# Kernel optimization log

Hardware: AMD Instinct MI355X
Metric: run time of the kernel (lower is better)

The kernel has to match this reference:

```python
import jax, jax.numpy as jnp
import numpy as np

N_NODES = 100000


def setup_inputs() -> dict:
    key = jax.random.key(0)
    k1, k2, k3, k4 = jax.random.split(key, 4)
    E = 1600000
    D_IN, D_OUT = 128, 128
    feat = jax.random.normal(k1, (N_NODES, D_IN), dtype=jnp.float32)
    src = jax.random.randint(k2, (E,), 0, N_NODES, dtype=jnp.int32)
    dst = jax.random.randint(k3, (E,), 0, N_NODES, dtype=jnp.int32)
    # xavier_uniform for weight [in, out]
    limit = float(np.sqrt(6.0 / (D_IN + D_OUT)))
    weight = jax.random.uniform(k4, (D_IN, D_OUT), dtype=jnp.float32,
                                minval=-limit, maxval=limit)
    bias = jnp.zeros((D_OUT,), dtype=jnp.float32)
    return {"feat": feat, "weight": weight, "bias": bias, "src": src, "dst": dst}


def reference(feat, weight, bias, src, dst):
    # in-degree normalization: norm_i = 1/sqrt(in_deg(i)); clamp deg>=1 to avoid inf
    deg = jax.ops.segment_sum(jnp.ones(src.shape[0], dtype=jnp.float32), dst,
                              num_segments=N_NODES)
    norm = jax.lax.rsqrt(jnp.maximum(deg, 1.0))[:, None]  # [N,1]
    h = feat * norm
    # update_all(copy_src, sum): scatter-sum src features into dst nodes (SpMM)
    agg = jax.ops.segment_sum(h[src], dst, num_segments=N_NODES)  # [N, D_in]
    # in_feats == out_feats -> aggregate first, then dense transform
    rst = agg @ weight          # [N, D_out]
    rst = rst * norm + bias
    return rst
```

## Files before the change

kernel.cpp:

```cpp
#include <hip/hip_runtime.h>


constexpr int N_NODES = 100000;
constexpr int D = 128;
constexpr int NB = 256;
constexpr int GROUP = (N_NODES + NB - 1) / NB;
constexpr int CAP = 14336;

typedef float f32x4 __attribute__((ext_vector_type(4)));
typedef short short8 __attribute__((ext_vector_type(8)));
typedef unsigned uint4v __attribute__((ext_vector_type(4)));

__device__ __forceinline__ ushort f2bf(float x) {
    unsigned u = __float_as_uint(x);
    return (ushort)((u + 0x7fffu + ((u >> 16) & 1u)) >> 16);
}
__device__ __forceinline__ float bf2f(ushort h) {
    return __uint_as_float(((unsigned)h) << 16);
}

__global__ __launch_bounds__(256) void p1_histo(const int* __restrict__ dst, int E,
                                                int* __restrict__ bhist) {
    __shared__ int h[NB];
    int t = threadIdx.x, blk = blockIdx.x;
    h[t] = 0; __syncthreads();
    int per = (E + NB - 1) / NB;
    int s = blk * per, e = min(E, s + per);
    for (int i = s + t; i < e; i += 256) atomicAdd(&h[dst[i] / GROUP], 1);
    __syncthreads();
    bhist[t * NB + blk] = h[t];
}

__global__ __launch_bounds__(256) void p1_scanrow(int* __restrict__ bhist,
                                                  int* __restrict__ rowtot) {
    __shared__ int lds[256];
    int b = blockIdx.x, t = threadIdx.x;
    int v = bhist[b * NB + t];
    lds[t] = v; __syncthreads();
    for (int off = 1; off < 256; off <<= 1) {
        int x = (t >= off) ? lds[t - off] : 0;
        __syncthreads();
        lds[t] += x;
        __syncthreads();
    }
    bhist[b * NB + t] = lds[t] - v;
    if (t == 255) rowtot[b] = lds[255];
}

__global__ __launch_bounds__(256) void p1_scantot(const int* __restrict__ rowtot,
                                                  int* __restrict__ bktBase) {
    __shared__ int lds[256];
    int t = threadIdx.x;
    int v = rowtot[t];
    lds[t] = v; __syncthreads();
    for (int off = 1; off < 256; off <<= 1) {
        int x = (t >= off) ? lds[t - off] : 0;
        __syncthreads();
        lds[t] += x;
        __syncthreads();
    }
    bktBase[t] = lds[t] - v;
    if (t == 255) bktBase[NB] = lds[255];
}

__global__ __launch_bounds__(256) void p1_scatter(const int* __restrict__ src,
                                                  const int* __restrict__ dst, int E,
                                                  const int* __restrict__ bhist,
                                                  const int* __restrict__ bktBase,
                                                  int* __restrict__ pairs) {
    __shared__ int loff[NB];
    int t = threadIdx.x, blk = blockIdx.x;
    loff[t] = bhist[t * NB + blk] + bktBase[t]; __syncthreads();
    int per = (E + NB - 1) / NB;
    int s = blk * per, e = min(E, s + per);
    for (int i = s + t; i < e; i += 256) {
        int d = dst[i];
        int b = d / GROUP;
        int pos = atomicAdd(&loff[b], 1);
        pairs[pos] = ((d - b * GROUP) << 17) | src[i];
    }
}

__global__ __launch_bounds__(256) void p2_degoffs(const int* __restrict__ pairs,
                                                  const int* __restrict__ bktBase,
                                                  int* __restrict__ deg,
                                                  int* __restrict__ offs,
                                                  float* __restrict__ norm) {
    __shared__ int h[512];
    __shared__ int ssum[256];
    int t = threadIdx.x, b = blockIdx.x;
    int lo = b * GROUP;
    int cnt = min(GROUP, N_NODES - lo);
    for (int i = t; i < 512; i += 256) h[i] = 0;
    __syncthreads();
    int s0 = bktBase[b], s1 = bktBase[b + 1];
    for (int i = s0 + t; i < s1; i += 256) atomicAdd(&h[pairs[i] >> 17], 1);
    __syncthreads();
    int v0 = h[2 * t], v1 = h[2 * t + 1];
    int s = v0 + v1;
    ssum[t] = s; __syncthreads();
    for (int off = 1; off < 256; off <<= 1) {
        int x = (t >= off) ? ssum[t - off] : 0;
        __syncthreads();
        ssum[t] += x;
        __syncthreads();
    }
    int pre = ssum[t] - s;
    if (2 * t < cnt) {
        int node = lo + 2 * t;
        deg[node] = v0;
        offs[node] = s0 + pre;
        norm[node] = rsqrtf(fmaxf((float)v0, 1.0f));
    }
    if (2 * t + 1 < cnt) {
        int node = lo + 2 * t + 1;
        deg[node] = v1;
        offs[node] = s0 + pre + v0;
        norm[node] = rsqrtf(fmaxf((float)v1, 1.0f));
    }
}

__global__ __launch_bounds__(256) void p2_scatter(const int* __restrict__ pairs,
                                                  const int* __restrict__ bktBase,
                                                  const int* __restrict__ offs, int E,
                                                  int* __restrict__ esrc) {
    __shared__ int loffs[GROUP];
    __shared__ int lcur[GROUP];
    __shared__ int sbuf[CAP];
    int t = threadIdx.x, b = blockIdx.x;
    int lo = b * GROUP;
    int cnt = min(GROUP, N_NODES - lo);
    int base = bktBase[b];
    int end  = bktBase[b + 1];
    int wsize = end - base;
    for (int i = t; i < cnt; i += 256) { loffs[i] = offs[lo + i] - base; lcur[i] = 0; }
    __syncthreads();
    bool fits = (wsize <= CAP);
    for (int i = base + t; i < end; i += 256) {
        int p = pairs[i];
        int dl = p >> 17;
        int sv = p & 0x1FFFF;
        int pos = loffs[dl] + atomicAdd(&lcur[dl], 1);
        if (fits) sbuf[pos] = sv; else esrc[base + pos] = sv;
    }
    __syncthreads();
    if (fits)
        for (int i = t; i < wsize; i += 256) esrc[base + i] = sbuf[i];
}

__global__ void k_featbf(const float* __restrict__ feat, const float* __restrict__ norm,
                         unsigned* __restrict__ ft, int total) {
    int i = blockIdx.x * blockDim.x + threadIdx.x;
    if (i < total) {
        float w = norm[i >> 6];
        float2 v = ((const float2*)feat)[i];
        ft[i] = (unsigned)f2bf(v.x * w) | ((unsigned)f2bf(v.y * w) << 16);
    }
}

template<bool OUT_BF>
__global__ __launch_bounds__(256) void k_gather4(const unsigned* __restrict__ ft,
                                                 const int* __restrict__ offs,
                                                 const int* __restrict__ deg,
                                                 const int* __restrict__ esrc,
                                                 void* __restrict__ out) {
    int gtid = blockIdx.x * blockDim.x + threadIdx.x;
    int node = gtid >> 6;
    if (node >= N_NODES) return;
    int lane = gtid & 63;
    int g  = lane >> 4;
    int sl = lane & 15;
    int start = offs[node];
    int cnt   = deg[node];
    int last  = start + cnt - 1;
    float acc[8] = {0.f, 0.f, 0.f, 0.f, 0.f, 0.f, 0.f, 0.f};
    const uint4v* ftv = (const uint4v*)ft;
    for (int j = 0; j < cnt; j += 4) {
        int idx = start + j + g;
        int s = esrc[min(idx, last)];
        float w = (j + g < cnt) ? 1.0f : 0.0f;
        uint4v u = ftv[(size_t)s * 16 + sl];
        #pragma unroll
        for (int q = 0; q < 4; ++q) {
            unsigned uu = u[q];
            acc[q * 2]     = fmaf(__uint_as_float(uu << 16),          w, acc[q * 2]);
            acc[q * 2 + 1] = fmaf(__uint_as_float(uu & 0xffff0000u),  w, acc[q * 2 + 1]);
        }
    }
    #pragma unroll
    for (int q = 0; q < 8; ++q) {
        acc[q] += __shfl_xor(acc[q], 16, 64);
        acc[q] += __shfl_xor(acc[q], 32, 64);
    }
    if (OUT_BF) {
        if (g == 0) {
            uint4v o;
            #pragma unroll
            for (int q = 0; q < 4; ++q)
                o[q] = (unsigned)f2bf(acc[q * 2]) | ((unsigned)f2bf(acc[q * 2 + 1]) << 16);
            ((uint4v*)out)[(size_t)node * 16 + sl] = o;
        }
    } else {
        float2 o = {acc[g * 2], acc[g * 2 + 1]};
        ((float2*)out)[(size_t)node * 64 + sl * 4 + g] = o;
    }
}

__global__ __launch_bounds__(256) void k_gather(const float* __restrict__ feat,
                                                const float* __restrict__ norm,
                                                const int* __restrict__ offs,
                                                const int* __restrict__ deg,
                                                const int* __restrict__ esrc,
                                                float* __restrict__ agg) {
    int gtid = blockIdx.x * blockDim.x + threadIdx.x;
    int node = gtid >> 6;
    int lane = gtid & 63;
    if (node >= N_NODES) return;
    int start = offs[node];
    int cnt   = deg[node];
    float2 acc = {0.f, 0.f};
    const float2* feat2 = (const float2*)feat;
    int j = 0;
    for (; j + 2 <= cnt; j += 2) {
        int s0 = esrc[start + j];
        int s1 = esrc[start + j + 1];
        float n0 = norm[s0], n1 = norm[s1];
        float2 v0 = feat2[(size_t)s0 * 64 + lane];
        float2 v1 = feat2[(size_t)s1 * 64 + lane];
        acc.x = fmaf(v0.x, n0, acc.x); acc.y = fmaf(v0.y, n0, acc.y);
        acc.x = fmaf(v1.x, n1, acc.x); acc.y = fmaf(v1.y, n1, acc.y);
    }
    if (j < cnt) {
        int s0 = esrc[start + j];
        float n0 = norm[s0];
        float2 v0 = feat2[(size_t)s0 * 64 + lane];
        acc.x = fmaf(v0.x, n0, acc.x); acc.y = fmaf(v0.y, n0, acc.y);
    }
    ((float2*)agg)[(size_t)node * 64 + lane] = acc;
}

__global__ void k_wpack(const float* __restrict__ W, ushort* __restrict__ whi,
                        ushort* __restrict__ wlo) {
    int p = blockIdx.x * blockDim.x + threadIdx.x;
    if (p >= 16384) return;
    int i  = p & 7;
    int l  = (p >> 3) & 63;
    int kt = (p >> 9) & 3;
    int ct = (p >> 11);
    int k = kt * 32 + (l >> 4) * 8 + i;
    int n = ct * 16 + (l & 15);
    float x = W[k * 128 + n];
    ushort h = f2bf(x);
    whi[p] = h;
    wlo[p] = f2bf(x - bf2f(h));
}

__global__ __launch_bounds__(256) void k_gemm_bf(const ushort* __restrict__ aggbf,
                                                 const ushort* __restrict__ whi,
                                                 const ushort* __restrict__ wlo,
                                                 const float* __restrict__ bias,
                                                 const float* __restrict__ norm,
                                                 float* __restrict__ out) {
    __shared__ ushort sH[16384];
    __shared__ ushort sL[16384];
    {
        const short8* gh = (const short8*)whi;
        const short8* gl = (const short8*)wlo;
        short8* lh = (short8*)sH;
        short8* ll = (short8*)sL;
        for (int i = threadIdx.x; i < 2048; i += 256) { lh[i] = gh[i]; ll[i] = gl[i]; }
    }
    __syncthreads();

    const int lane = threadIdx.x & 63;
    const int wid  = threadIdx.x >> 6;
    const int rsub = lane & 15;
    const int kgrp = lane >> 4;

    const short8* BH = (const short8*)sH;
    const short8* BL = (const short8*)sL;

    const int nstrips = N_NODES / 16;
    for (int strip = blockIdx.x * 4 + wid; strip < nstrips; strip += gridDim.x * 4) {
        const int row0 = strip * 16;
        const ushort* arow = aggbf + (size_t)(row0 + rsub) * D + kgrp * 8;
        short8 a[4];
        #pragma unroll
        for (int kt = 0; kt < 4; ++kt) a[kt] = *(const short8*)(arow + kt * 32);
        float nr[4];
        #pragma unroll
        for (int r = 0; r < 4; ++r) nr[r] = norm[row0 + kgrp * 4 + r];

        #pragma unroll
        for (int ct = 0; ct < 8; ++ct) {
            f32x4 acc = {0.f, 0.f, 0.f, 0.f};
            #pragma unroll
            for (int kt = 0; kt < 4; ++kt) {
                acc = __builtin_amdgcn_mfma_f32_16x16x32_bf16(a[kt], BH[(ct * 4 + kt) * 64 + lane], acc, 0, 0, 0);
                acc = __builtin_amdgcn_mfma_f32_16x16x32_bf16(a[kt], BL[(ct * 4 + kt) * 64 + lane], acc, 0, 0, 0);
            }
            const float bc = bias[ct * 16 + rsub];
            float* ocol = out + (size_t)row0 * D + ct * 16 + rsub;
            #pragma unroll
            for (int r = 0; r < 4; ++r) {
                int row = kgrp * 4 + r;
                ocol[(size_t)row * D] = acc[r] * nr[r] + bc;
            }
        }
    }
}

__global__ __launch_bounds__(256) void k_gemm_mfma(float* __restrict__ io,
                                                   const ushort* __restrict__ whi,
                                                   const ushort* __restrict__ wlo,
                                                   const float* __restrict__ bias,
                                                   const float* __restrict__ norm) {
    __shared__ ushort sH[16384];
    __shared__ ushort sL[16384];
    {
        const short8* gh = (const short8*)whi;
        const short8* gl = (const short8*)wlo;
        short8* lh = (short8*)sH;
        short8* ll = (short8*)sL;
        for (int i = threadIdx.x; i < 2048; i += 256) { lh[i] = gh[i]; ll[i] = gl[i]; }
    }
    __syncthreads();

    const int lane = threadIdx.x & 63;
    const int wid  = threadIdx.x >> 6;
    const int rsub = lane & 15;
    const int kgrp = lane >> 4;

    const short8* BH = (const short8*)sH;
    const short8* BL = (const short8*)sL;

    const int nstrips = N_NODES / 16;
    for (int strip = blockIdx.x * 4 + wid; strip < nstrips; strip += gridDim.x * 4) {
        const int row0 = strip * 16;
        const float* arow = io + (size_t)(row0 + rsub) * D + kgrp * 8;
        short8 ahi[4], alo[4];
        #pragma unroll
        for (int kt = 0; kt < 4; ++kt) {
            f32x4 x0 = *(const f32x4*)(arow + kt * 32);
            f32x4 x1 = *(const f32x4*)(arow + kt * 32 + 4);
            short8 h, l;
            #pragma unroll
            for (int j = 0; j < 4; ++j) {
                ushort h0 = f2bf(x0[j]);
                h[j]     = (short)h0;  l[j]     = (short)f2bf(x0[j] - bf2f(h0));
                ushort h1 = f2bf(x1[j]);
                h[j + 4] = (short)h1;  l[j + 4] = (short)f2bf(x1[j] - bf2f(h1));
            }
            ahi[kt] = h; alo[kt] = l;
        }
        float nr[4];
        #pragma unroll
        for (int r = 0; r < 4; ++r) nr[r] = norm[row0 + kgrp * 4 + r];

        #pragma unroll
        for (int ct = 0; ct < 8; ++ct) {
            f32x4 acc = {0.f, 0.f, 0.f, 0.f};
            #pragma unroll
            for (int kt = 0; kt < 4; ++kt) {
                short8 bh = BH[(ct * 4 + kt) * 64 + lane];
                short8 bl = BL[(ct * 4 + kt) * 64 + lane];
                acc = __builtin_amdgcn_mfma_f32_16x16x32_bf16(ahi[kt], bh, acc, 0, 0, 0);
                acc = __builtin_amdgcn_mfma_f32_16x16x32_bf16(alo[kt], bh, acc, 0, 0, 0);
                acc = __builtin_amdgcn_mfma_f32_16x16x32_bf16(ahi[kt], bl, acc, 0, 0, 0);
            }
            const float bc = bias[ct * 16 + rsub];
            float* ocol = io + (size_t)row0 * D + ct * 16 + rsub;
            #pragma unroll
            for (int r = 0; r < 4; ++r) {
                int row = kgrp * 4 + r;
                ocol[(size_t)row * D] = acc[r] * nr[r] + bc;
            }
        }
    }
}

__global__ void k_scatter(const float* __restrict__ feat, const int* __restrict__ src,
                          const int* __restrict__ dst, const float* __restrict__ norm,
                          int E, float* __restrict__ agg) {
    long long gtid = (long long)blockIdx.x * blockDim.x + threadIdx.x;
    int e    = (int)(gtid >> 6);
    int lane = (int)(gtid & 63);
    if (e >= E) return;
    int s = src[e];
    int t = dst[e];
    float ns = norm[s];
    float2 v = ((const float2*)(feat + (size_t)s * D))[lane];
    float* arow = agg + (size_t)t * D + lane * 2;
    atomicAdd(arow + 0, v.x * ns);
    atomicAdd(arow + 1, v.y * ns);
}
__global__ void k_deg_f(const int* __restrict__ dst, int E, float* __restrict__ deg) {
    int i = blockIdx.x * blockDim.x + threadIdx.x;
    if (i < E) atomicAdd(deg + dst[i], 1.0f);
}
__global__ void k_norm_f(float* __restrict__ dn) {
    int i = blockIdx.x * blockDim.x + threadIdx.x;
    if (i < N_NODES) dn[i] = rsqrtf(fmaxf(dn[i], 1.0f));
}
__global__ __launch_bounds__(256) void k_gemm(float* __restrict__ io,
                                              const float* __restrict__ W,
                                              const float* __restrict__ bias,
                                              const float* __restrict__ norm) {
    __shared__ float sW[D * D];
    __shared__ float srow[2][D];
    for (int i = threadIdx.x; i < D * D; i += 256) sW[i] = W[i];
    const int r = threadIdx.x >> 7;
    const int c = threadIdx.x & 127;
    const float bc = bias[c];
    const int npairs = N_NODES / 2;
    for (int rp = blockIdx.x; rp < npairs; rp += gridDim.x) {
        __syncthreads();
        const int row = rp * 2 + r;
        srow[r][c] = io[(size_t)row * D + c];
        __syncthreads();
        float acc = 0.f;
        #pragma unroll 8
        for (int k = 0; k < D; ++k)
            acc = fmaf(srow[r][k], sW[k * D + c], acc);
        io[(size_t)row * D + c] = acc * norm[row] + bc;
    }
}

extern "C" void kernel_launch(void* const* d_in, const int* in_sizes, int n_in,
                              void* d_out, int out_size, void* d_ws, size_t ws_size,
                              hipStream_t stream) {
    const float* feat   = (const float*)d_in[0];
    const float* weight = (const float*)d_in[1];
    const float* bias   = (const float*)d_in[2];
    const int*   src    = (const int*)d_in[3];
    const int*   dst    = (const int*)d_in[4];
    const int E = in_sizes[3];

    float* agg   = (float*)d_out;
    int*   pairs = (int*)d_out;

    uintptr_t cur = (uintptr_t)d_ws;
    auto take = [&](size_t bytes) -> void* {
        uintptr_t r = (cur + 63) & ~(uintptr_t)63;
        cur = r + bytes;
        return (void*)r;
    };

    size_t S_ft   = (size_t)N_NODES * 64 * 4;
    size_t S_agg  = (size_t)N_NODES * D * 2;
    size_t S_small = (size_t)(3 * N_NODES + 256 + NB * NB + NB + 1 + E) * 4 + 65536 + 16 * 64;
    size_t needB  = S_small;
    size_t needA  = S_small + S_ft + 64;
    size_t needA2 = needA + S_agg + 64;

    bool tierA2 = ws_size >= needA2;
    bool tierA  = ws_size >= needA;
    bool tierB  = ws_size >= needB;

    unsigned* ft    = (tierA || tierA2) ? (unsigned*)take(S_ft) : nullptr;
    ushort*   aggbf = tierA2 ? (ushort*)take(S_agg) : nullptr;
    float*    norm    = (float*)take((size_t)N_NODES * 4);
    int*      deg     = (int*)take((size_t)N_NODES * 4);
    int*      offs    = (int*)take((size_t)N_NODES * 4);
    int*      rowtot  = (int*)take(256 * 4);
    int*      bhist   = (int*)take((size_t)NB * NB * 4);
    int*      bktBase = (int*)take((size_t)(NB + 1) * 4);
    int*      esrc    = (int*)take((size_t)E * 4);
    ushort*   whi     = (ushort*)take(16384 * 2);
    ushort*   wlo     = (ushort*)take(16384 * 2);

    if (tierB) {
        k_wpack<<<64, 256, 0, stream>>>(weight, whi, wlo);
        p1_histo<<<NB, 256, 0, stream>>>(dst, E, bhist);
        p1_scanrow<<<NB, 256, 0, stream>>>(bhist, rowtot);
        p1_scantot<<<1, 256, 0, stream>>>(rowtot, bktBase);
        p1_scatter<<<NB, 256, 0, stream>>>(src, dst, E, bhist, bktBase, pairs);
        p2_degoffs<<<NB, 256, 0, stream>>>(pairs, bktBase, deg, offs, norm);
        p2_scatter<<<NB, 256, 0, stream>>>(pairs, bktBase, offs, E, esrc);

        long long gthreads = (long long)N_NODES * 64;
        int gblocks = (int)((gthreads + 255) / 256);
        if (tierA || tierA2) {
            k_featbf<<<(N_NODES * 64 + 255) / 256, 256, 0, stream>>>(feat, norm, ft, N_NODES * 64);
            if (tierA2) {
                k_gather4<true><<<gblocks, 256, 0, stream>>>(ft, offs, deg, esrc, aggbf);
                k_gemm_bf<<<1024, 256, 0, stream>>>(aggbf, whi, wlo, bias, norm, (float*)d_out);
            } else {
                k_gather4<false><<<gblocks, 256, 0, stream>>>(ft, offs, deg, esrc, agg);
                k_gemm_mfma<<<1024, 256, 0, stream>>>(agg, whi, wlo, bias, norm);
            }
        } else {
            k_gather<<<gblocks, 256, 0, stream>>>(feat, norm, offs, deg, esrc, agg);
            k_gemm_mfma<<<1024, 256, 0, stream>>>(agg, whi, wlo, bias, norm);
        }
    } else {
        hipMemsetAsync(d_out, 0, (size_t)N_NODES * D * sizeof(float), stream);
        hipMemsetAsync(norm, 0, (size_t)N_NODES * sizeof(float), stream);
        k_deg_f<<<(E + 255) / 256, 256, 0, stream>>>(dst, E, (float*)norm);
        k_norm_f<<<(N_NODES + 255) / 256, 256, 0, stream>>>((float*)norm);
        long long sthreads = (long long)E * 64;
        k_scatter<<<(int)((sthreads + 255) / 256), 256, 0, stream>>>(feat, src, dst, norm, E, agg);
        k_gemm<<<4096, 256, 0, stream>>>(agg, weight, bias, norm);
    }
}
```

Baseline: 160.7 us.

## Fuse preprocessing kernels, merge scan into consumers, and unroll gather by eight

Folds weight packing into the histogram kernel and drops the separate total-scan kernel, so each consumer recomputes the 256-entry bucket prefix itself. Merges the degree/offset and CSR scatter kernels into one pass that reuses the local prefix as atomic cursors. The feature bf16 conversion now handles four floats per thread, and the gather loop processes two edges per group per iteration for more memory-level parallelism. This cuts kernel-launch count and the re-reads of pairs, at the cost of redundant small scans per block and more shared memory in the merged kernel, which may lower occupancy.

```diff
diff --git a/kernel.cpp b/kernel.cpp
--- a/kernel.cpp
+++ b/kernel.cpp
@@ -20,10 +20,27 @@
 }
 
 __global__ __launch_bounds__(256) void p1_histo(const int* __restrict__ dst, int E,
-                                                int* __restrict__ bhist) {
+                                                int* __restrict__ bhist,
+                                                const float* __restrict__ W,
+                                                ushort* __restrict__ whi,
+                                                ushort* __restrict__ wlo) {
     __shared__ int h[NB];
     int t = threadIdx.x, blk = blockIdx.x;
-    h[t] = 0; __syncthreads();
+    h[t] = 0;
+    if (blk < 64) {
+        int p = blk * 256 + t;
+        int i  = p & 7;
+        int l  = (p >> 3) & 63;
+        int kt = (p >> 9) & 3;
+        int ct = (p >> 11);
+        int k = kt * 32 + (l >> 4) * 8 + i;
+        int n = ct * 16 + (l & 15);
+        float x = W[k * 128 + n];
+        ushort hh = f2bf(x);
+        whi[p] = hh;
+        wlo[p] = f2bf(x - bf2f(hh));
+    }
+    __syncthreads();
     int per = (E + NB - 1) / NB;
     int s = blk * per, e = min(E, s + per);
     for (int i = s + t; i < e; i += 256) atomicAdd(&h[dst[i] / GROUP], 1);
@@ -47,30 +64,24 @@
     if (t == 255) rowtot[b] = lds[255];
 }
 
-__global__ __launch_bounds__(256) void p1_scantot(const int* __restrict__ rowtot,
-                                                  int* __restrict__ bktBase) {
-    __shared__ int lds[256];
-    int t = threadIdx.x;
-    int v = rowtot[t];
-    lds[t] = v; __syncthreads();
-    for (int off = 1; off < 256; off <<= 1) {
-        int x = (t >= off) ? lds[t - off] : 0;
-        __syncthreads();
-        lds[t] += x;
-        __syncthreads();
-    }
-    bktBase[t] = lds[t] - v;
-    if (t == 255) bktBase[NB] = lds[255];
-}
-
 __global__ __launch_bounds__(256) void p1_scatter(const int* __restrict__ src,
                                                   const int* __restrict__ dst, int E,
                                                   const int* __restrict__ bhist,
-                                                  const int* __restrict__ bktBase,
+                                                  const int* __restrict__ rowtot,
                                                   int* __restrict__ pairs) {
     __shared__ int loff[NB];
+    __shared__ int bb[NB];
     int t = threadIdx.x, blk = blockIdx.x;
-    loff[t] = bhist[t * NB + blk] + bktBase[t]; __syncthreads();
+    int rv = rowtot[t];
+    bb[t] = rv; __syncthreads();
+    for (int off = 1; off < 256; off <<= 1) {
+        int x = (t >= off) ? bb[t - off] : 0;
+        __syncthreads();
+        bb[t] += x;
+        __syncthreads();
+    }
+    loff[t] = bhist[t * NB + blk] + bb[t] - rv;
+    __syncthreads();
     int per = (E + NB - 1) / NB;
     int s = blk * per, e = min(E, s + per);
     for (int i = s + t; i < e; i += 256) {
@@ -81,21 +92,37 @@
     }
 }
 
-__global__ __launch_bounds__(256) void p2_degoffs(const int* __restrict__ pairs,
-                                                  const int* __restrict__ bktBase,
-                                                  int* __restrict__ deg,
-                                                  int* __restrict__ offs,
-                                                  float* __restrict__ norm) {
+__global__ __launch_bounds__(256) void p2_all(const int* __restrict__ pairs,
+                                              const int* __restrict__ rowtot,
+                                              int* __restrict__ deg,
+                                              int* __restrict__ offs,
+                                              float* __restrict__ norm,
+                                              int* __restrict__ esrc) {
     __shared__ int h[512];
     __shared__ int ssum[256];
+    __shared__ int bb[256];
+    __shared__ int sbuf[CAP];
     int t = threadIdx.x, b = blockIdx.x;
     int lo = b * GROUP;
     int cnt = min(GROUP, N_NODES - lo);
-    for (int i = t; i < 512; i += 256) h[i] = 0;
-    __syncthreads();
-    int s0 = bktBase[b], s1 = bktBase[b + 1];
+
+    int rv = rowtot[t];
+    bb[t] = rv;
+    h[t] = 0; h[t + 256] = 0;
+    __syncthreads();
+    for (int off = 1; off < 256; off <<= 1) {
+        int x = (t >= off) ? bb[t - off] : 0;
+        __syncthreads();
+        bb[t] += x;
+        __syncthreads();
+    }
+    int s1 = bb[b];
+    int s0 = s1 - rowtot[b];
+    __syncthreads();
+
     for (int i = s0 + t; i < s1; i += 256) atomicAdd(&h[pairs[i] >> 17], 1);
     __syncthreads();
+
     int v0 = h[2 * t], v1 = h[2 * t + 1];
     int s = v0 + v1;
     ssum[t] = s; __syncthreads();
@@ -118,52 +145,43 @@
         offs[node] = s0 + pre + v0;
         norm[node] = rsqrtf(fmaxf((float)v1, 1.0f));
     }
-}
-
-__global__ __launch_bounds__(256) void p2_scatter(const int* __restrict__ pairs,
-                                                  const int* __restrict__ bktBase,
-                                                  const int* __restrict__ offs, int E,
-                                                  int* __restrict__ esrc) {
-    __shared__ int loffs[GROUP];
-    __shared__ int lcur[GROUP];
-    __shared__ int sbuf[CAP];
-    int t = threadIdx.x, b = blockIdx.x;
-    int lo = b * GROUP;
-    int cnt = min(GROUP, N_NODES - lo);
-    int base = bktBase[b];
-    int end  = bktBase[b + 1];
-    int wsize = end - base;
-    for (int i = t; i < cnt; i += 256) { loffs[i] = offs[lo + i] - base; lcur[i] = 0; }
-    __syncthreads();
+    __syncthreads();
+    h[2 * t] = pre;
+    h[2 * t + 1] = pre + v0;
+    __syncthreads();
+
+    int wsize = s1 - s0;
     bool fits = (wsize <= CAP);
-    for (int i = base + t; i < end; i += 256) {
+    for (int i = s0 + t; i < s1; i += 256) {
         int p = pairs[i];
         int dl = p >> 17;
         int sv = p & 0x1FFFF;
-        int pos = loffs[dl] + atomicAdd(&lcur[dl], 1);
-        if (fits) sbuf[pos] = sv; else esrc[base + pos] = sv;
+        int pos = atomicAdd(&h[dl], 1);
+        if (fits) sbuf[pos] = sv; else esrc[s0 + pos] = sv;
     }
     __syncthreads();
     if (fits)
-        for (int i = t; i < wsize; i += 256) esrc[base + i] = sbuf[i];
+        for (int i = t; i < wsize; i += 256) esrc[s0 + i] = sbuf[i];
 }
 
 __global__ void k_featbf(const float* __restrict__ feat, const float* __restrict__ norm,
-                         unsigned* __restrict__ ft, int total) {
+                         uint2* __restrict__ ft2, int total) {
     int i = blockIdx.x * blockDim.x + threadIdx.x;
     if (i < total) {
-        float w = norm[i >> 6];
-        float2 v = ((const float2*)feat)[i];
-        ft[i] = (unsigned)f2bf(v.x * w) | ((unsigned)f2bf(v.y * w) << 16);
-    }
-}
-
-template<bool OUT_BF>
-__global__ __launch_bounds__(256) void k_gather4(const unsigned* __restrict__ ft,
+        float w = norm[i >> 5];
+        f32x4 v = ((const f32x4*)feat)[i];
+        uint2 o;
+        o.x = (unsigned)f2bf(v[0] * w) | ((unsigned)f2bf(v[1] * w) << 16);
+        o.y = (unsigned)f2bf(v[2] * w) | ((unsigned)f2bf(v[3] * w) << 16);
+        ft2[i] = o;
+    }
+}
+
+__global__ __launch_bounds__(256) void k_gather8(const unsigned* __restrict__ ft,
                                                  const int* __restrict__ offs,
                                                  const int* __restrict__ deg,
                                                  const int* __restrict__ esrc,
-                                                 void* __restrict__ out) {
+                                                 unsigned* __restrict__ outbf) {
     int gtid = blockIdx.x * blockDim.x + threadIdx.x;
     int node = gtid >> 6;
     if (node >= N_NODES) return;
@@ -175,16 +193,26 @@
     int last  = start + cnt - 1;
     float acc[8] = {0.f, 0.f, 0.f, 0.f, 0.f, 0.f, 0.f, 0.f};
     const uint4v* ftv = (const uint4v*)ft;
-    for (int j = 0; j < cnt; j += 4) {
-        int idx = start + j + g;
-        int s = esrc[min(idx, last)];
-        float w = (j + g < cnt) ? 1.0f : 0.0f;
-        uint4v u = ftv[(size_t)s * 16 + sl];
+    for (int j = 0; j < cnt; j += 8) {
+        int i0 = start + j + g;
+        int i1 = start + j + 4 + g;
+        int s0v = esrc[min(i0, last)];
+        int s1v = esrc[min(i1, last)];
+        float w0 = (j + g     < cnt) ? 1.0f : 0.0f;
+        float w1 = (j + 4 + g < cnt) ? 1.0f : 0.0f;
+        uint4v u0 = ftv[(size_t)s0v * 16 + sl];
+        uint4v u1 = ftv[(size_t)s1v * 16 + sl];
         #pragma unroll
         for (int q = 0; q < 4; ++q) {
-            unsigned uu = u[q];
-            acc[q * 2]     = fmaf(__uint_as_float(uu << 16),          w, acc[q * 2]);
-            acc[q * 2 + 1] = fmaf(__uint_as_float(uu & 0xffff0000u),  w, acc[q * 2 + 1]);
+            unsigned a = u0[q];
+            acc[q * 2]     = fmaf(__uint_as_float(a << 16),         w0, acc[q * 2]);
+            acc[q * 2 + 1] = fmaf(__uint_as_float(a & 0xffff0000u), w0, acc[q * 2 + 1]);
+        }
+        #pragma unroll
+        for (int q = 0; q < 4; ++q) {
+            unsigned a = u1[q];
+            acc[q * 2]     = fmaf(__uint_as_float(a << 16),         w1, acc[q * 2]);
+            acc[q * 2 + 1] = fmaf(__uint_as_float(a & 0xffff0000u), w1, acc[q * 2 + 1]);
         }
     }
     #pragma unroll
@@ -192,67 +220,13 @@
         acc[q] += __shfl_xor(acc[q], 16, 64);
         acc[q] += __shfl_xor(acc[q], 32, 64);
     }
-    if (OUT_BF) {
-        if (g == 0) {
-            uint4v o;
-            #pragma unroll
-            for (int q = 0; q < 4; ++q)
-                o[q] = (unsigned)f2bf(acc[q * 2]) | ((unsigned)f2bf(acc[q * 2 + 1]) << 16);
-            ((uint4v*)out)[(size_t)node * 16 + sl] = o;
-        }
-    } else {
-        float2 o = {acc[g * 2], acc[g * 2 + 1]};
-        ((float2*)out)[(size_t)node * 64 + sl * 4 + g] = o;
-    }
-}
-
-__global__ __launch_bounds__(256) void k_gather(const float* __restrict__ feat,
-                                                const float* __restrict__ norm,
-                                                const int* __restrict__ offs,
-                                                const int* __restrict__ deg,
-                                                const int* __restrict__ esrc,
-                                                float* __restrict__ agg) {
-    int gtid = blockIdx.x * blockDim.x + threadIdx.x;
-    int node = gtid >> 6;
-    int lane = gtid & 63;
-    if (node >= N_NODES) return;
-    int start = offs[node];
-    int cnt   = deg[node];
-    float2 acc = {0.f, 0.f};
-    const float2* feat2 = (const float2*)feat;
-    int j = 0;
-    for (; j + 2 <= cnt; j += 2) {
-        int s0 = esrc[start + j];
-        int s1 = esrc[start + j + 1];
-        float n0 = norm[s0], n1 = norm[s1];
-        float2 v0 = feat2[(size_t)s0 * 64 + lane];
-        float2 v1 = feat2[(size_t)s1 * 64 + lane];
-        acc.x = fmaf(v0.x, n0, acc.x); acc.y = fmaf(v0.y, n0, acc.y);
-        acc.x = fmaf(v1.x, n1, acc.x); acc.y = fmaf(v1.y, n1, acc.y);
-    }
-    if (j < cnt) {
-        int s0 = esrc[start + j];
-        float n0 = norm[s0];
-        float2 v0 = feat2[(size_t)s0 * 64 + lane];
-        acc.x = fmaf(v0.x, n0, acc.x); acc.y = fmaf(v0.y, n0, acc.y);
-    }
-    ((float2*)agg)[(size_t)node * 64 + lane] = acc;
-}
-
-__global__ void k_wpack(const float* __restrict__ W, ushort* __restrict__ whi,
-                        ushort* __restrict__ wlo) {
-    int p = blockIdx.x * blockDim.x + threadIdx.x;
-    if (p >= 16384) return;
-    int i  = p & 7;
-    int l  = (p >> 3) & 63;
-    int kt = (p >> 9) & 3;
-    int ct = (p >> 11);
-    int k = kt * 32 + (l >> 4) * 8 + i;
-    int n = ct * 16 + (l & 15);
-    float x = W[k * 128 + n];
-    ushort h = f2bf(x);
-    whi[p] = h;
-    wlo[p] = f2bf(x - bf2f(h));
+    if (g == 0) {
+        uint4v o;
+        #pragma unroll
+        for (int q = 0; q < 4; ++q)
+            o[q] = (unsigned)f2bf(acc[q * 2]) | ((unsigned)f2bf(acc[q * 2 + 1]) << 16);
+        ((uint4v*)outbf)[(size_t)node * 16 + sl] = o;
+    }
 }
 
 __global__ __launch_bounds__(256) void k_gemm_bf(const ushort* __restrict__ aggbf,
@@ -310,75 +284,6 @@
     }
 }
 
-__global__ __launch_bounds__(256) void k_gemm_mfma(float* __restrict__ io,
-                                                   const ushort* __restrict__ whi,
-                                                   const ushort* __restrict__ wlo,
-                                                   const float* __restrict__ bias,
-                                                   const float* __restrict__ norm) {
-    __shared__ ushort sH[16384];
-    __shared__ ushort sL[16384];
-    {
-        const short8* gh = (const short8*)whi;
-        const short8* gl = (const short8*)wlo;
-        short8* lh = (short8*)sH;
-        short8* ll = (short8*)sL;
-        for (int i = threadIdx.x; i < 2048; i += 256) { lh[i] = gh[i]; ll[i] = gl[i]; }
-    }
-    __syncthreads();
-
-    const int lane = threadIdx.x & 63;
-    const int wid  = threadIdx.x >> 6;
-    const int rsub = lane & 15;
-    const int kgrp = lane >> 4;
-
-    const short8* BH = (const short8*)sH;
-    const short8* BL = (const short8*)sL;
-
-    const int nstrips = N_NODES / 16;
-    for (int strip = blockIdx.x * 4 + wid; strip < nstrips; strip += gridDim.x * 4) {
-        const int row0 = strip * 16;
-        const float* arow = io + (size_t)(row0 + rsub) * D + kgrp * 8;
-        short8 ahi[4], alo[4];
-        #pragma unroll
-        for (int kt = 0; kt < 4; ++kt) {
-            f32x4 x0 = *(const f32x4*)(arow + kt * 32);
-            f32x4 x1 = *(const f32x4*)(arow + kt * 32 + 4);
-            short8 h, l;
-            #pragma unroll
-            for (int j = 0; j < 4; ++j) {
-                ushort h0 = f2bf(x0[j]);
-                h[j]     = (short)h0;  l[j]     = (short)f2bf(x0[j] - bf2f(h0));
-                ushort h1 = f2bf(x1[j]);
-                h[j + 4] = (short)h1;  l[j + 4] = (short)f2bf(x1[j] - bf2f(h1));
-            }
-            ahi[kt] = h; alo[kt] = l;
-        }
-        float nr[4];
-        #pragma unroll
-        for (int r = 0; r < 4; ++r) nr[r] = norm[row0 + kgrp * 4 + r];
-
-        #pragma unroll
-        for (int ct = 0; ct < 8; ++ct) {
-            f32x4 acc = {0.f, 0.f, 0.f, 0.f};
-            #pragma unroll
-            for (int kt = 0; kt < 4; ++kt) {
-                short8 bh = BH[(ct * 4 + kt) * 64 + lane];
-                short8 bl = BL[(ct * 4 + kt) * 64 + lane];
-                acc = __builtin_amdgcn_mfma_f32_16x16x32_bf16(ahi[kt], bh, acc, 0, 0, 0);
-                acc = __builtin_amdgcn_mfma_f32_16x16x32_bf16(alo[kt], bh, acc, 0, 0, 0);
-                acc = __builtin_amdgcn_mfma_f32_16x16x32_bf16(ahi[kt], bl, acc, 0, 0, 0);
-            }
-            const float bc = bias[ct * 16 + rsub];
-            float* ocol = io + (size_t)row0 * D + ct * 16 + rsub;
-            #pragma unroll
-            for (int r = 0; r < 4; ++r) {
-                int row = kgrp * 4 + r;
-                ocol[(size_t)row * D] = acc[r] * nr[r] + bc;
-            }
-        }
-    }
-}
-
 __global__ void k_scatter(const float* __restrict__ feat, const int* __restrict__ src,
                           const int* __restrict__ dst, const float* __restrict__ norm,
                           int E, float* __restrict__ agg) {
@@ -436,8 +341,7 @@
     const int*   dst    = (const int*)d_in[4];
     const int E = in_sizes[3];
 
-    float* agg   = (float*)d_out;
-    int*   pairs = (int*)d_out;
+    int* pairs = (int*)d_out;
 
     uintptr_t cur = (uintptr_t)d_ws;
     auto take = [&](size_t bytes) -> void* {
@@ -446,60 +350,39 @@
         return (void*)r;
     };
 
-    size_t S_ft   = (size_t)N_NODES * 64 * 4;
-    size_t S_agg  = (size_t)N_NODES * D * 2;
-    size_t S_small = (size_t)(3 * N_NODES + 256 + NB * NB + NB + 1 + E) * 4 + 65536 + 16 * 64;
-    size_t needB  = S_small;
-    size_t needA  = S_small + S_ft + 64;
-    size_t needA2 = needA + S_agg + 64;
-
-    bool tierA2 = ws_size >= needA2;
-    bool tierA  = ws_size >= needA;
-    bool tierB  = ws_size >= needB;
-
-    unsigned* ft    = (tierA || tierA2) ? (unsigned*)take(S_ft) : nullptr;
-    ushort*   aggbf = tierA2 ? (ushort*)take(S_agg) : nullptr;
-    float*    norm    = (float*)take((size_t)N_NODES * 4);
-    int*      deg     = (int*)take((size_t)N_NODES * 4);
-    int*      offs    = (int*)take((size_t)N_NODES * 4);
-    int*      rowtot  = (int*)take(256 * 4);
-    int*      bhist   = (int*)take((size_t)NB * NB * 4);
-    int*      bktBase = (int*)take((size_t)(NB + 1) * 4);
-    int*      esrc    = (int*)take((size_t)E * 4);
-    ushort*   whi     = (ushort*)take(16384 * 2);
-    ushort*   wlo     = (ushort*)take(16384 * 2);
-
-    if (tierB) {
-        k_wpack<<<64, 256, 0, stream>>>(weight, whi, wlo);
-        p1_histo<<<NB, 256, 0, stream>>>(dst, E, bhist);
+    size_t S_ft  = (size_t)N_NODES * 64 * 4;
+    size_t S_agg = (size_t)N_NODES * D * 2;
+    size_t need  = S_ft + S_agg +
+                   (size_t)(3 * N_NODES + 256 + NB * NB + E) * 4 + 65536 + 1024;
+
+    unsigned* ft     = (unsigned*)take(S_ft);
+    ushort*   aggbf  = (ushort*)take(S_agg);
+    float*    norm   = (float*)take((size_t)N_NODES * 4);
+    int*      deg    = (int*)take((size_t)N_NODES * 4);
+    int*      offs   = (int*)take((size_t)N_NODES * 4);
+    int*      rowtot = (int*)take(256 * 4);
+    int*      bhist  = (int*)take((size_t)NB * NB * 4);
+    int*      esrc   = (int*)take((size_t)E * 4);
+    ushort*   whi    = (ushort*)take(16384 * 2);
+    ushort*   wlo    = (ushort*)take(16384 * 2);
+
+    if (ws_size >= need) {
+        p1_histo<<<NB, 256, 0, stream>>>(dst, E, bhist, weight, whi, wlo);
         p1_scanrow<<<NB, 256, 0, stream>>>(bhist, rowtot);
-        p1_scantot<<<1, 256, 0, stream>>>(rowtot, bktBase);
-        p1_scatter<<<NB, 256, 0, stream>>>(src, dst, E, bhist, bktBase, pairs);
-        p2_degoffs<<<NB, 256, 0, stream>>>(pairs, bktBase, deg, offs, norm);
-        p2_scatter<<<NB, 256, 0, stream>>>(pairs, bktBase, offs, E, esrc);
-
+        p1_scatter<<<NB, 256, 0, stream>>>(src, dst, E, bhist, rowtot, pairs);
+        p2_all<<<NB, 256, 0, stream>>>(pairs, rowtot, deg, offs, norm, esrc);
+        k_featbf<<<(N_NODES * 32 + 255) / 256, 256, 0, stream>>>(feat, norm, (uint2*)ft, N_NODES * 32);
         long long gthreads = (long long)N_NODES * 64;
-        int gblocks = (int)((gthreads + 255) / 256);
-        if (tierA || tierA2) {
-            k_featbf<<<(N_NODES * 64 + 255) / 256, 256, 0, stream>>>(feat, norm, ft, N_NODES * 64);
-            if (tierA2) {
-                k_gather4<true><<<gblocks, 256, 0, stream>>>(ft, offs, deg, esrc, aggbf);
-                k_gemm_bf<<<1024, 256, 0, stream>>>(aggbf, whi, wlo, bias, norm, (float*)d_out);
-            } else {
-                k_gather4<false><<<gblocks, 256, 0, stream>>>(ft, offs, deg, esrc, agg);
-                k_gemm_mfma<<<1024, 256, 0, stream>>>(agg, whi, wlo, bias, norm);
-            }
-        } else {
-            k_gather<<<gblocks, 256, 0, stream>>>(feat, norm, offs, deg, esrc, agg);
-            k_gemm_mfma<<<1024, 256, 0, stream>>>(agg, whi, wlo, bias, norm);
-        }
+        k_gather8<<<(int)((gthreads + 255) / 256), 256, 0, stream>>>(ft, offs, deg, esrc, (unsigned*)aggbf);
+        k_gemm_bf<<<1024, 256, 0, stream>>>(aggbf, whi, wlo, bias, norm, (float*)d_out);
     } else {
+        float* agg = (float*)d_out;
         hipMemsetAsync(d_out, 0, (size_t)N_NODES * D * sizeof(float), stream);
         hipMemsetAsync(norm, 0, (size_t)N_NODES * sizeof(float), stream);
         k_deg_f<<<(E + 255) / 256, 256, 0, stream>>>(dst, E, (float*)norm);
         k_norm_f<<<(N_NODES + 255) / 256, 256, 0, stream>>>((float*)norm);
         long long sthreads = (long long)E * 64;
-        k_scatter<<<(int)((sthreads + 255) / 256), 256, 0, stream>>>(feat, src, dst, norm, E, agg);
-        k_gemm<<<4096, 256, 0, stream>>>(agg, weight, bias, norm);
-    }
-}
+        k_scatter<<<(int)((sthreads + 255) / 256), 256, 0, stream>>>(feat, src, dst, (float*)norm, E, agg);
+        k_gemm<<<4096, 256, 0, stream>>>(agg, weight, bias, (float*)norm);
+    }
+}
```

After: 140.9 us. 1.14x faster.
